# Optimization experiments

Measured on AMD Instinct MI355X. Metric: run time of the kernel, lower is better.

Reference implementation:

```python
import jax, jax.numpy as jnp
import numpy as np

THRESHOLD = 0.0

def setup_inputs() -> dict:
    key = jax.random.key(0)
    k1, k2 = jax.random.split(key)
    B, N, D = 16384, 16384, 128
    query_embeddings = jax.random.normal(k1, (B, D), dtype=jnp.float32)
    # module normalizes learned centroids; emulate for provided centroids too-faithfulness
    # NOTE: forward itself does NOT normalize provided cluster_embeddings, so we pass raw randn
    cluster_embeddings = jax.random.normal(k2, (N, D), dtype=jnp.float32)
    return {"query_embeddings": query_embeddings,
            "cluster_embeddings": cluster_embeddings,
            "top_k": 8}

def reference(query_embeddings, cluster_embeddings, top_k):
    # cosine similarity path: plain matmul (B, N)
    all_similarities = jnp.matmul(query_embeddings, cluster_embeddings.T)
    k = min(int(top_k), all_similarities.shape[1])
    top_k_similarities, top_k_indices = jax.lax.top_k(all_similarities, k)
    mask = top_k_similarities >= THRESHOLD
    cluster_ids = jnp.where(mask, top_k_indices, -1)
    return (cluster_ids, top_k_similarities, all_similarities)
```

## Files before the change

### kernel.cpp

```cpp
#include <hip/hip_runtime.h>
#include <math.h>

#define NROWS 16384
#define NCOLS 16384
#define DIM   128
#define TM    128
#define TN    64
#define NSPLIT 4
#define CPS   (NCOLS/NSPLIT)
#define NCH   (CPS/TN)
#define NMACRO (NCH/2)
#define KP    16
#define BOUNCE 16384u

typedef __attribute__((ext_vector_type(8))) short bf16x8;
typedef __attribute__((ext_vector_type(4))) float f32x4;

__device__ __forceinline__ unsigned short bf16_rne(float x) {
  unsigned u = __float_as_uint(x);
  unsigned r = u + 0x7fffu + ((u >> 16) & 1u);
  return (unsigned short)(r >> 16);
}

__device__ __forceinline__ unsigned mkkey(float v, int col) {
  unsigned b = __float_as_uint(v);
  unsigned u = b ^ (unsigned)(((int)b >> 31) | (int)0x80000000);
  return (u & 0xFFFFC000u) | (unsigned)(16383 - col);
}

#define INSERT(tk, key) do {                                                  \
  unsigned _k = (key);                                                        \
  if (_k > tk[KP - 1]) {                                                      \
    tk[KP - 1] = _k;                                                          \
    _Pragma("unroll")                                                         \
    for (int _m = KP - 1; _m > 0; --_m)                                       \
      if (tk[_m] > tk[_m - 1]) {                                              \
        unsigned _q = tk[_m]; tk[_m] = tk[_m - 1]; tk[_m - 1] = _q;           \
      }                                                                       \
  }                                                                           \
} while (0)

#define BAR() do {                                   \
  __builtin_amdgcn_sched_barrier(0);                 \
  asm volatile("s_waitcnt lgkmcnt(0)" ::: "memory"); \
  __builtin_amdgcn_s_barrier();                      \
  __builtin_amdgcn_sched_barrier(0);                 \
} while (0)

__global__ __launch_bounds__(256) void split_kernel(
    const float* __restrict__ C, unsigned char* __restrict__ Cimg)
{
  const unsigned u = blockIdx.x * 256 + threadIdx.x;
  const int c  = u & 16383;
  const int kk = u >> 14;
  const f32x4* src = (const f32x4*)(C + (size_t)c * DIM + kk * 16);
  f32x4 f[4];
  f[0] = src[0]; f[1] = src[1]; f[2] = src[2]; f[3] = src[3];
  const unsigned chunkbase = ((unsigned)(c >> 6)) << 14;
  const unsigned T = ((((unsigned)c >> 4) & 3u) << 2) | ((unsigned)kk >> 1);
  #pragma unroll
  for (int s = 0; s < 2; ++s) {
    bf16x8 h;
    #pragma unroll
    for (int e = 0; e < 8; ++e)
      h[e] = (short)bf16_rne(f[s * 2 + (e >> 2)][e & 3]);
    unsigned ln = (unsigned)(c & 15) | ((((unsigned)kk * 2 + s) & 3u) << 4);
    *(bf16x8*)&Cimg[chunkbase + (T << 10) + (ln << 4)] = h;
  }
}

__global__ __launch_bounds__(512, 4) void sim_topk_kernel(
    const float* __restrict__ Q, const unsigned char* __restrict__ Cimg,
    float* __restrict__ S, int* __restrict__ cand)
{
  __shared__ __align__(16) unsigned char lds[81920];
  const int t = threadIdx.x;
  const int w = t >> 6, lane = t & 63;

  const int bid = blockIdx.x;
  const int xcd = bid & 7;
  const int cs  = xcd >> 1;
  const int rb  = ((xcd & 1) << 6) | (bid >> 3);
  const int row0 = rb * TM;
  const int col0 = cs * CPS;
  const int mphase = rb & (NMACRO - 1);

  const int arow = row0 + w * 16 + (lane & 15);
  bf16x8 a_h[4];
  {
    const f32x4* Qp = (const f32x4*)(Q + (size_t)arow * DIM) + (lane >> 4) * 2;
    #pragma unroll
    for (int ks = 0; ks < 4; ++ks) {
      f32x4 x0 = Qp[ks * 8], x1 = Qp[ks * 8 + 1];
      #pragma unroll
      for (int e = 0; e < 8; ++e)
        a_h[ks][e] = (short)bf16_rne((e < 4) ? x0[e & 3] : x1[e & 3]);
    }
  }

  f32x4 st0, st1, st2, st3;
  auto gload01 = [&](int ch) {
    const f32x4* p = (const f32x4*)(Cimg + (((size_t)(cs * NCH + ch)) << 14)) + t;
    st0 = p[0]; st1 = p[512];
  };
  auto gload23 = [&](int ch) {
    const f32x4* p = (const f32x4*)(Cimg + (((size_t)(cs * NCH + ch)) << 14)) + t;
    st2 = p[0]; st3 = p[512];
  };
  auto swriteB01 = [&]() {
    *(f32x4*)&lds[(unsigned)t * 16u]         = st0;
    *(f32x4*)&lds[8192u + (unsigned)t * 16u] = st1;
  };
  auto swriteB23 = [&]() {
    *(f32x4*)&lds[(unsigned)t * 16u]         = st2;
    *(f32x4*)&lds[8192u + (unsigned)t * 16u] = st3;
  };

  {
    const int mch0 = mphase;
    gload01(mch0 * 2);
    gload23(mch0 * 2 + 1);
  }

  unsigned tk[KP];
  #pragma unroll
  for (int j = 0; j < KP; ++j) tk[j] = 0u;

  const int rloc = w * 16 + (lane & 15);
  const unsigned rswz = (unsigned)(rloc & 7);

  for (int m = 0; m < NMACRO; ++m) {
    const int mch = (mphase + m) & (NMACRO - 1);
    const int colbase = col0 + mch * 128;

    #pragma unroll
    for (int half = 0; half < 2; ++half) {
      if (half == 0) swriteB01(); else swriteB23();
      if (half == 1 && m + 1 < NMACRO) {
        const int nm = (mphase + m + 1) & (NMACRO - 1);
        gload01(nm * 2);
        gload23(nm * 2 + 1);
      }
      BAR();

      f32x4 acc[4];
      #pragma unroll
      for (int c = 0; c < 4; ++c) acc[c] = {0.f, 0.f, 0.f, 0.f};
      #pragma unroll
      for (int ks = 0; ks < 4; ++ks) {
        #pragma unroll
        for (int ct = 0; ct < 4; ++ct) {
          unsigned o = ((unsigned)(ct * 4 + ks) << 10) + ((unsigned)lane << 4);
          bf16x8 bh = *(const bf16x8*)&lds[o];
          acc[ct] = __builtin_amdgcn_mfma_f32_16x16x32_bf16(bh, a_h[ks], acc[ct], 0, 0, 0);
        }
      }

      const int hc = colbase + half * 64;
      #pragma unroll
      for (int ct = 0; ct < 4; ++ct) {
        const int c16 = half * 16 + ct * 4 + (lane >> 4);
        unsigned baddr = BOUNCE + (unsigned)rloc * 512u +
                         (((unsigned)c16 ^ rswz) << 4);
        *(f32x4*)&lds[baddr] = acc[ct];
        const int cg = hc + ct * 16 + (lane >> 4) * 4;
        #pragma unroll
        for (int e = 0; e < 4; ++e)
          INSERT(tk, mkkey(acc[ct][e], cg + e));
      }
      BAR();
    }

    {
      const int cql = lane & 31;
      #pragma unroll
      for (int d = 0; d < 8; ++d) {
        const int row = w * 16 + d * 2 + (lane >> 5);
        unsigned baddr = BOUNCE + (unsigned)row * 512u +
                         (((unsigned)cql ^ (unsigned)(row & 7)) << 4);
        f32x4 v = *(const f32x4*)&lds[baddr];
        *(f32x4*)&S[(size_t)(row0 + row) * NCOLS + colbase + cql * 4] = v;
      }
    }
    BAR();
  }

  #pragma unroll
  for (int off = 16; off <= 32; off <<= 1) {
    unsigned ov[KP];
    #pragma unroll
    for (int j = 0; j < KP; ++j)
      ov[j] = (unsigned)__shfl_xor((int)tk[j], off);
    #pragma unroll
    for (int j = 0; j < KP; ++j) INSERT(tk, ov[j]);
  }
  if (lane < 16) {
    int* dst = cand + ((size_t)(row0 + w * 16 + lane) * NSPLIT + cs) * KP;
    #pragma unroll
    for (int j = 0; j < KP; ++j) dst[j] = 16383 - (int)(tk[j] & 0x3FFFu);
  }
}

__global__ __launch_bounds__(256) void rerank_kernel(
    const float* __restrict__ Q, const float* __restrict__ C,
    const int* __restrict__ cand, float* __restrict__ out)
{
  const int t = threadIdx.x, w = t >> 6, lane = t & 63;
  const int r = blockIdx.x * 4 + w;
  const f32x4* Q4 = (const f32x4*)(Q + (size_t)r * DIM);

  const int cidx = cand[(size_t)r * (NSPLIT * KP) + lane];
  const f32x4* C4 = (const f32x4*)(C + (size_t)cidx * DIM);

  double acc = 0.0;
  #pragma unroll 8
  for (int d4 = 0; d4 < 32; ++d4) {
    f32x4 q = Q4[d4];
    f32x4 c = C4[d4];
    acc += (double)q[0] * (double)c[0];
    acc += (double)q[1] * (double)c[1];
    acc += (double)q[2] * (double)c[2];
    acc += (double)q[3] * (double)c[3];
  }

  double mv = acc;
  int    mi = cidx;

  float* oi = out;
  float* os = out + (size_t)NROWS * 8;

  for (int k = 0; k < 8; ++k) {
    double bv = mv; int bi = mi;
    #pragma unroll
    for (int off = 32; off >= 1; off >>= 1) {
      double ov = __shfl_xor(bv, off);
      int    o2 = __shfl_xor(bi, off);
      if (ov > bv || (ov == bv && o2 < bi)) { bv = ov; bi = o2; }
    }
    if (lane == 0) {
      os[(size_t)r * 8 + k] = (float)bv;
      oi[(size_t)r * 8 + k] = (bv >= 0.0) ? (float)bi : -1.0f;
    }
    if (mi == bi) mv = -1.0e300;
  }
}

extern "C" void kernel_launch(void* const* d_in, const int* in_sizes, int n_in,
                              void* d_out, int out_size, void* d_ws, size_t ws_size,
                              hipStream_t stream) {
  const float* Q = (const float*)d_in[0];
  const float* C = (const float*)d_in[1];
  float* out = (float*)d_out;
  float* S   = out + (size_t)2 * NROWS * 8;

  unsigned char* Cimg = (unsigned char*)d_ws;
  int* cand = (int*)(Cimg + 4194304);

  split_kernel<<<dim3(512), dim3(256), 0, stream>>>(C, Cimg);
  sim_topk_kernel<<<dim3((NROWS / TM) * NSPLIT), dim3(512), 0, stream>>>(Q, Cimg, S, cand);
  rerank_kernel<<<dim3(NROWS / 4), dim3(256), 0, stream>>>(Q, C, cand, out);
}
```

Measured before the change: 507.8 us.

## Load B fragments straight into registers per wave and drop block barriers

```diff
diff --git a/kernel.cpp b/kernel.cpp
--- a/kernel.cpp
+++ b/kernel.cpp
@@ -11,7 +11,6 @@
 #define NCH   (CPS/TN)
 #define NMACRO (NCH/2)
 #define KP    16
-#define BOUNCE 16384u
 
 typedef __attribute__((ext_vector_type(8))) short bf16x8;
 typedef __attribute__((ext_vector_type(4))) float f32x4;
@@ -38,13 +37,6 @@
         unsigned _q = tk[_m]; tk[_m] = tk[_m - 1]; tk[_m - 1] = _q;           \
       }                                                                       \
   }                                                                           \
-} while (0)
-
-#define BAR() do {                                   \
-  __builtin_amdgcn_sched_barrier(0);                 \
-  asm volatile("s_waitcnt lgkmcnt(0)" ::: "memory"); \
-  __builtin_amdgcn_s_barrier();                      \
-  __builtin_amdgcn_sched_barrier(0);                 \
 } while (0)
 
 __global__ __launch_bounds__(256) void split_kernel(
@@ -73,7 +65,7 @@
     const float* __restrict__ Q, const unsigned char* __restrict__ Cimg,
     float* __restrict__ S, int* __restrict__ cand)
 {
-  __shared__ __align__(16) unsigned char lds[81920];
+  __shared__ __align__(16) unsigned char lds[65536];
   const int t = threadIdx.x;
   const int w = t >> 6, lane = t & 63;
 
@@ -83,7 +75,8 @@
   const int rb  = ((xcd & 1) << 6) | (bid >> 3);
   const int row0 = rb * TM;
   const int col0 = cs * CPS;
-  const int mphase = rb & (NMACRO - 1);
+  const int wphase = ((rb << 3) | w) & (NMACRO - 1);
+  unsigned char* bounce = lds + (unsigned)w * 8192u;
 
   const int arow = row0 + w * 16 + (lane & 15);
   bf16x8 a_h[4];
@@ -98,50 +91,34 @@
     }
   }
 
-  f32x4 st0, st1, st2, st3;
-  auto gload01 = [&](int ch) {
-    const f32x4* p = (const f32x4*)(Cimg + (((size_t)(cs * NCH + ch)) << 14)) + t;
-    st0 = p[0]; st1 = p[512];
+  bf16x8 b0[16], b1[16];
+  auto gload = [&](bf16x8* dst, int ch) {
+    const bf16x8* p = (const bf16x8*)(Cimg + (((size_t)(cs * NCH + ch)) << 14));
+    #pragma unroll
+    for (int T = 0; T < 16; ++T) dst[T] = p[(T << 6) + lane];
   };
-  auto gload23 = [&](int ch) {
-    const f32x4* p = (const f32x4*)(Cimg + (((size_t)(cs * NCH + ch)) << 14)) + t;
-    st2 = p[0]; st3 = p[512];
-  };
-  auto swriteB01 = [&]() {
-    *(f32x4*)&lds[(unsigned)t * 16u]         = st0;
-    *(f32x4*)&lds[8192u + (unsigned)t * 16u] = st1;
-  };
-  auto swriteB23 = [&]() {
-    *(f32x4*)&lds[(unsigned)t * 16u]         = st2;
-    *(f32x4*)&lds[8192u + (unsigned)t * 16u] = st3;
-  };
-
-  {
-    const int mch0 = mphase;
-    gload01(mch0 * 2);
-    gload23(mch0 * 2 + 1);
-  }
+
+  gload(b0, wphase * 2);
 
   unsigned tk[KP];
   #pragma unroll
   for (int j = 0; j < KP; ++j) tk[j] = 0u;
 
-  const int rloc = w * 16 + (lane & 15);
-  const unsigned rswz = (unsigned)(rloc & 7);
+  const int r16 = lane & 15;
+  const unsigned rswz = (unsigned)(r16 & 7);
 
   for (int m = 0; m < NMACRO; ++m) {
-    const int mch = (mphase + m) & (NMACRO - 1);
+    const int mch = (wphase + m) & (NMACRO - 1);
     const int colbase = col0 + mch * 128;
 
     #pragma unroll
     for (int half = 0; half < 2; ++half) {
-      if (half == 0) swriteB01(); else swriteB23();
-      if (half == 1 && m + 1 < NMACRO) {
-        const int nm = (mphase + m + 1) & (NMACRO - 1);
-        gload01(nm * 2);
-        gload23(nm * 2 + 1);
-      }
-      BAR();
+      if (half == 0) {
+        gload(b1, mch * 2 + 1);
+      } else if (m + 1 < NMACRO) {
+        gload(b0, ((wphase + m + 1) & (NMACRO - 1)) * 2);
+      }
+      const bf16x8* bcur = half ? b1 : b0;
 
       f32x4 acc[4];
       #pragma unroll
@@ -149,40 +126,33 @@
       #pragma unroll
       for (int ks = 0; ks < 4; ++ks) {
         #pragma unroll
-        for (int ct = 0; ct < 4; ++ct) {
-          unsigned o = ((unsigned)(ct * 4 + ks) << 10) + ((unsigned)lane << 4);
-          bf16x8 bh = *(const bf16x8*)&lds[o];
-          acc[ct] = __builtin_amdgcn_mfma_f32_16x16x32_bf16(bh, a_h[ks], acc[ct], 0, 0, 0);
-        }
+        for (int ct = 0; ct < 4; ++ct)
+          acc[ct] = __builtin_amdgcn_mfma_f32_16x16x32_bf16(
+                        bcur[ct * 4 + ks], a_h[ks], acc[ct], 0, 0, 0);
       }
 
       const int hc = colbase + half * 64;
       #pragma unroll
       for (int ct = 0; ct < 4; ++ct) {
         const int c16 = half * 16 + ct * 4 + (lane >> 4);
-        unsigned baddr = BOUNCE + (unsigned)rloc * 512u +
-                         (((unsigned)c16 ^ rswz) << 4);
-        *(f32x4*)&lds[baddr] = acc[ct];
+        *(f32x4*)&bounce[(unsigned)r16 * 512u + (((unsigned)c16 ^ rswz) << 4)] = acc[ct];
         const int cg = hc + ct * 16 + (lane >> 4) * 4;
         #pragma unroll
         for (int e = 0; e < 4; ++e)
           INSERT(tk, mkkey(acc[ct][e], cg + e));
       }
-      BAR();
     }
 
     {
       const int cql = lane & 31;
       #pragma unroll
       for (int d = 0; d < 8; ++d) {
-        const int row = w * 16 + d * 2 + (lane >> 5);
-        unsigned baddr = BOUNCE + (unsigned)row * 512u +
-                         (((unsigned)cql ^ (unsigned)(row & 7)) << 4);
-        f32x4 v = *(const f32x4*)&lds[baddr];
-        *(f32x4*)&S[(size_t)(row0 + row) * NCOLS + colbase + cql * 4] = v;
-      }
-    }
-    BAR();
+        const int rr = d * 2 + (lane >> 5);
+        f32x4 v = *(const f32x4*)&bounce[(unsigned)rr * 512u +
+                       (((unsigned)cql ^ (unsigned)(rr & 7)) << 4)];
+        *(f32x4*)&S[(size_t)(row0 + w * 16 + rr) * NCOLS + colbase + cql * 4] = v;
+      }
+    }
   }
 
   #pragma unroll
```

Result: slower. 1.101 ms (+116.9%).
